# Kernel optimization log

Hardware: AMD Instinct MI355X
Metric: run time of the kernel (lower is better)

Reference implementation:

```python
import jax, jax.numpy as jnp
import numpy as np

N_EMBD = 768
N_HEAD = 12
N_KV_HEAD = 4                      # repeat factor in _repeat_kv
NUM_KV_HEADS = N_HEAD // N_KV_HEAD # 3 actual kv heads
HEAD_DIM = N_EMBD // N_HEAD        # 64
BLOCK_SIZE = 1024                  # sliding window size
SCALE = (HEAD_DIM * N_KV_HEAD / N_HEAD) ** (-0.5)


def _rotary_cos_sin(T, d, dtype):
    inv_freq = 1.0 / (10000.0 ** (jnp.arange(0, d, 2, dtype=jnp.float32) / d))
    t = jnp.arange(T, dtype=jnp.float32)
    freqs = jnp.outer(t, inv_freq)  # (T, d/2)
    return jnp.cos(freqs).astype(dtype)[None, None], jnp.sin(freqs).astype(dtype)[None, None]


def _apply_rotary(x):
    # x: (b, h, T, d)
    T, d = x.shape[2], x.shape[3]
    cos, sin = _rotary_cos_sin(T, d, x.dtype)
    x1, x2 = x[..., : d // 2], x[..., d // 2 :]
    return jnp.concatenate([x1 * cos - x2 * sin, x1 * sin + x2 * cos], axis=-1)


def setup_inputs() -> dict:
    key = jax.random.key(0)
    k0, k1, k2, k3, k4 = jax.random.split(key, 5)
    b, T = 2, 2048
    s = 0.02
    return {
        "hidden_states": jax.random.normal(k0, (b, T, N_EMBD), jnp.float32),
        "Wq": jax.random.normal(k1, (N_HEAD * HEAD_DIM, N_EMBD), jnp.float32) * s,
        "Wk": jax.random.normal(k2, (NUM_KV_HEADS * HEAD_DIM, N_EMBD), jnp.float32) * s,
        "Wv": jax.random.normal(k3, (NUM_KV_HEADS * HEAD_DIM, N_EMBD), jnp.float32) * s,
        "Wo": jax.random.normal(k4, (N_EMBD, N_HEAD * HEAD_DIM), jnp.float32) * s,
    }


def reference(hidden_states, Wq, Wk, Wv, Wo):
    b, T, _ = hidden_states.shape
    q = (hidden_states @ Wq.T).reshape(b, T, N_HEAD, HEAD_DIM).transpose(0, 2, 1, 3)
    k = (hidden_states @ Wk.T).reshape(b, T, NUM_KV_HEADS, HEAD_DIM).transpose(0, 2, 1, 3)
    v = (hidden_states @ Wv.T).reshape(b, T, NUM_KV_HEADS, HEAD_DIM).transpose(0, 2, 1, 3)

    # _repeat_kv: each kv head repeated n_kv_head (=4) times contiguously
    k = jnp.repeat(k, N_KV_HEAD, axis=1)
    v = jnp.repeat(v, N_KV_HEAD, axis=1)

    q = _apply_rotary(q)
    k = _apply_rotary(k)

    # centered sliding-window mask (faithful to per-token loop):
    # window_start = clip(i - W//2, 0, T - W); window is always exactly W wide
    W = BLOCK_SIZE
    i = jnp.arange(T)[:, None]
    j = jnp.arange(T)[None, :]
    start = jnp.clip(i - W // 2, 0, T - W)
    mask = (j >= start) & (j < start + W)  # (T, T)

    scores = jnp.einsum("bhqd,bhkd->bhqk", q, k) * SCALE
    scores = jnp.where(mask[None, None], scores, jnp.finfo(scores.dtype).min)
    attn = jax.nn.softmax(scores, axis=-1)
    out = jnp.einsum("bhqk,bhkd->bhqd", attn, v)  # (b, h, T, d)

    out = out.transpose(0, 2, 1, 3).reshape(b, T, N_EMBD)
    return out @ Wo.T
```

## Files before the change

### kernel.cpp

```cpp
#include <hip/hip_runtime.h>
#include <math.h>

#define T_SEQ 2048
#define E 768
#define WIN 1024
#define KDIM 768
#define HS_SZ ((size_t)4096 * 768)
#define SCALE 0.21650635094610965f

typedef _Float16 f16x8 __attribute__((ext_vector_type(8)));
typedef _Float16 f16x4 __attribute__((ext_vector_type(4)));
typedef float f32x4 __attribute__((ext_vector_type(4)));
typedef __attribute__((address_space(3))) _Float16 lf16;

#define MFMA16(a, b, c) __builtin_amdgcn_mfma_f32_16x16x32_f16(a, b, c, 0, 0, 0)

__device__ __forceinline__ void dma16(const _Float16* g, lf16* l) {
    __builtin_amdgcn_global_load_lds(
        (const __attribute__((address_space(1))) void*)g,
        (__attribute__((address_space(3))) void*)l, 16, 0, 0);
}

__device__ __forceinline__ void cast8(const float* __restrict__ src,
                                      _Float16* __restrict__ dst, int i) {
    float4 a = *(const float4*)&src[i];
    float4 b = *(const float4*)&src[i + 4];
    f16x8 h;
    h[0] = (_Float16)a.x; h[1] = (_Float16)a.y; h[2] = (_Float16)a.z; h[3] = (_Float16)a.w;
    h[4] = (_Float16)b.x; h[5] = (_Float16)b.y; h[6] = (_Float16)b.z; h[7] = (_Float16)b.w;
    *(f16x8*)&dst[i] = h;
}

__global__ __launch_bounds__(256) void prep(
    const float* __restrict__ hs,
    const float* __restrict__ Wq, const float* __restrict__ Wk,
    const float* __restrict__ Wv, const float* __restrict__ Wo,
    _Float16* __restrict__ hs16,
    _Float16* __restrict__ Wq16, _Float16* __restrict__ Wk16,
    _Float16* __restrict__ Wv16, _Float16* __restrict__ Wo16,
    float2* __restrict__ rtab) {
    int tid = blockIdx.x * 256 + threadIdx.x;
    int i = tid * 8;
    if (i < 768 * 768) { cast8(Wq, Wq16, i); cast8(Wo, Wo16, i); }
    if (i < 192 * 768) { cast8(Wk, Wk16, i); cast8(Wv, Wv16, i); }
    cast8(hs, hs16, i);
    if (tid < 2048 * 32) {
        int t = tid >> 5, d = tid & 31;
        float inv = powf(10000.0f, -(float)(2 * d) * (1.0f / 64.0f));
        float s, c;
        sincosf((float)t * inv, &s, &c);
        rtab[tid] = make_float2(c, s);
    }
}

__global__ __launch_bounds__(256) void gemm_qkv(
    const _Float16* __restrict__ A16,
    const _Float16* __restrict__ Wq16, const _Float16* __restrict__ Wk16,
    const _Float16* __restrict__ Wv16, const float2* __restrict__ rtab,
    _Float16* __restrict__ q16, _Float16* __restrict__ k16,
    _Float16* __restrict__ vT16) {
    __shared__ __align__(16) _Float16 As[128 * 128];
    __shared__ __align__(16) _Float16 Bs[64 * 128];
    const int tid = threadIdx.x;
    const int bx = blockIdx.x;
    const int m0 = blockIdx.y * 128;
    const int w = tid >> 6, lane = tid & 63;
    const int mm = lane & 15, quad = lane >> 4;

    const _Float16* bbase; int brb;
    if (bx < 12)      { bbase = Wq16; brb = bx * 64; }
    else if (bx < 15) { bbase = Wk16; brb = (bx - 12) * 64; }
    else              { bbase = Wv16; brb = (bx - 15) * 64; }

    const int rofs4 = lane >> 4;
    const int gs = lane & 15;

    const _Float16* agp[8]; lf16* alp[8];
    #pragma unroll
    for (int j = 0; j < 8; ++j) {
        int c = j * 4 + w;
        int rr = c * 4 + rofs4;
        int glog = gs ^ (rr & 15);
        agp[j] = A16 + (size_t)(m0 + rr) * KDIM + glog * 8;
        alp[j] = ((lf16*)As) + c * 512 + lane * 8;
    }
    const _Float16* bgp[4]; lf16* blp[4];
    #pragma unroll
    for (int j = 0; j < 4; ++j) {
        int c = j * 4 + w;
        int rr = c * 4 + rofs4;
        int glog = gs ^ (rr & 15);
        bgp[j] = bbase + (size_t)(brb + rr) * KDIM + glog * 8;
        blp[j] = ((lf16*)Bs) + c * 512 + lane * 8;
    }

    f32x4 acc[2][4] = {};

    for (int it = 0; it < 6; ++it) {
        const int ke = it * 128;
        __syncthreads();
        #pragma unroll
        for (int j = 0; j < 8; ++j) dma16(agp[j] + ke, alp[j]);
        #pragma unroll
        for (int j = 0; j < 4; ++j) dma16(bgp[j] + ke, blp[j]);
        __syncthreads();
        #pragma unroll
        for (int s = 0; s < 4; ++s) {
            const int gq = ((s * 4 + quad) ^ mm) * 8;
            f16x8 ah[2];
            #pragma unroll
            for (int mt = 0; mt < 2; ++mt)
                ah[mt] = *(const f16x8*)&As[(w * 32 + mt * 16 + mm) * 128 + gq];
            #pragma unroll
            for (int nt = 0; nt < 4; ++nt) {
                f16x8 bh = *(const f16x8*)&Bs[(nt * 16 + mm) * 128 + gq];
                #pragma unroll
                for (int mt = 0; mt < 2; ++mt)
                    acc[mt][nt] = MFMA16(ah[mt], bh, acc[mt][nt]);
            }
        }
    }

    if (bx < 12) {
        #pragma unroll
        for (int mt = 0; mt < 2; ++mt)
            #pragma unroll
            for (int r = 0; r < 4; ++r) {
                int row = m0 + w * 32 + mt * 16 + quad * 4 + r;
                int t = row & (T_SEQ - 1);
                _Float16* dst = &q16[(size_t)row * E + bx * 64 + mm];
                #pragma unroll
                for (int nt = 0; nt < 2; ++nt) {
                    int d = nt * 16 + mm;
                    float2 cs = rtab[t * 32 + d];
                    float x1 = acc[mt][nt][r], x2 = acc[mt][nt + 2][r];
                    dst[nt * 16]       = (_Float16)((x1 * cs.x - x2 * cs.y) * SCALE);
                    dst[(nt + 2) * 16] = (_Float16)((x1 * cs.y + x2 * cs.x) * SCALE);
                }
            }
    } else if (bx < 15) {
        int kvh = bx - 12;
        #pragma unroll
        for (int mt = 0; mt < 2; ++mt)
            #pragma unroll
            for (int r = 0; r < 4; ++r) {
                int row = m0 + w * 32 + mt * 16 + quad * 4 + r;
                int t = row & (T_SEQ - 1);
                int b = row >> 11;
                _Float16* dst = &k16[(((size_t)(b * 3 + kvh)) * T_SEQ + t) * 64 + mm];
                #pragma unroll
                for (int nt = 0; nt < 2; ++nt) {
                    int d = nt * 16 + mm;
                    float2 cs = rtab[t * 32 + d];
                    float x1 = acc[mt][nt][r], x2 = acc[mt][nt + 2][r];
                    dst[nt * 16]       = (_Float16)(x1 * cs.x - x2 * cs.y);
                    dst[(nt + 2) * 16] = (_Float16)(x1 * cs.y + x2 * cs.x);
                }
            }
    } else {
        __syncthreads();
        _Float16 (*vs)[136] = (_Float16 (*)[136])As;
        #pragma unroll
        for (int mt = 0; mt < 2; ++mt)
            #pragma unroll
            for (int nt = 0; nt < 4; ++nt) {
                f16x4 pv;
                #pragma unroll
                for (int r = 0; r < 4; ++r) pv[r] = (_Float16)acc[mt][nt][r];
                *(f16x4*)&vs[nt * 16 + mm][w * 32 + mt * 16 + quad * 4] = pv;
            }
        __syncthreads();
        const int kvh = bx - 15;
        const int b = m0 >> 11, tbase = m0 & (T_SEQ - 1);
        const int tl = (tid & 15) * 8;
        #pragma unroll
        for (int j = 0; j < 4; ++j) {
            int dd = (tid >> 4) + j * 16;
            f16x8 vv = *(const f16x8*)&vs[dd][tl];
            *(f16x8*)&vT16[(((size_t)(b * 3 + kvh)) * 64 + dd) * T_SEQ + tbase + tl] = vv;
        }
    }
}

__global__ __launch_bounds__(256) void gemm_out(
    const _Float16* __restrict__ A16, const _Float16* __restrict__ B16,
    float* __restrict__ C) {
    __shared__ __align__(16) _Float16 As[128 * 128];
    __shared__ __align__(16) _Float16 Bs[64 * 128];
    const int tid = threadIdx.x;
    const int n0 = blockIdx.x * 64;
    const int m0 = blockIdx.y * 128;
    const int w = tid >> 6, lane = tid & 63;
    const int mm = lane & 15, quad = lane >> 4;

    const int rofs4 = lane >> 4;
    const int gs = lane & 15;

    const _Float16* agp[8]; lf16* alp[8];
    #pragma unroll
    for (int j = 0; j < 8; ++j) {
        int c = j * 4 + w;
        int rr = c * 4 + rofs4;
        int glog = gs ^ (rr & 15);
        agp[j] = A16 + (size_t)(m0 + rr) * KDIM + glog * 8;
        alp[j] = ((lf16*)As) + c * 512 + lane * 8;
    }
    const _Float16* bgp[4]; lf16* blp[4];
    #pragma unroll
    for (int j = 0; j < 4; ++j) {
        int c = j * 4 + w;
        int rr = c * 4 + rofs4;
        int glog = gs ^ (rr & 15);
        bgp[j] = B16 + (size_t)(n0 + rr) * KDIM + glog * 8;
        blp[j] = ((lf16*)Bs) + c * 512 + lane * 8;
    }

    f32x4 acc[2][4] = {};

    for (int it = 0; it < 6; ++it) {
        const int ke = it * 128;
        __syncthreads();
        #pragma unroll
        for (int j = 0; j < 8; ++j) dma16(agp[j] + ke, alp[j]);
        #pragma unroll
        for (int j = 0; j < 4; ++j) dma16(bgp[j] + ke, blp[j]);
        __syncthreads();
        #pragma unroll
        for (int s = 0; s < 4; ++s) {
            const int gq = ((s * 4 + quad) ^ mm) * 8;
            f16x8 ah[2];
            #pragma unroll
            for (int mt = 0; mt < 2; ++mt)
                ah[mt] = *(const f16x8*)&As[(w * 32 + mt * 16 + mm) * 128 + gq];
            #pragma unroll
            for (int nt = 0; nt < 4; ++nt) {
                f16x8 bh = *(const f16x8*)&Bs[(nt * 16 + mm) * 128 + gq];
                #pragma unroll
                for (int mt = 0; mt < 2; ++mt)
                    acc[mt][nt] = MFMA16(ah[mt], bh, acc[mt][nt]);
            }
        }
    }

    #pragma unroll
    for (int mt = 0; mt < 2; ++mt)
        #pragma unroll
        for (int r = 0; r < 4; ++r) {
            int row = m0 + w * 32 + mt * 16 + quad * 4 + r;
            float* cp = &C[(size_t)row * 768 + n0 + mm];
            #pragma unroll
            for (int nt = 0; nt < 4; ++nt)
                cp[nt * 16] = acc[mt][nt][r];
        }
}

__global__ __launch_bounds__(256) void attn_mfma(const _Float16* __restrict__ q16,
                                                 const _Float16* __restrict__ k16,
                                                 const _Float16* __restrict__ vT16,
                                                 _Float16* __restrict__ aout16) {
    __shared__ __align__(16) char smem[32768 + 10240];
    _Float16* k_s  = (_Float16*)smem;
    _Float16* vT_s = (_Float16*)(smem + 16384);
    _Float16 (*p_s)[40] = (_Float16(*)[40])(smem + 32768);
    float* ored = (float*)smem;
    float* lred = (float*)(smem + 16384);

    const int b = blockIdx.z, h = blockIdx.y;
    const int i0 = blockIdx.x * 64;
    const int plane = b * 3 + (h >> 2);
    const int tid = threadIdx.x;
    const int w = tid >> 6, lane = tid & 63;
    const int m = lane & 15, quad = lane >> 4;
    const int qh = w & 1, kh = w >> 1;
    const int xm = m & 7;

    int s0 = i0 - 512;      s0 = s0 < 0 ? 0 : (s0 > 1024 ? 1024 : s0);
    int sL = i0 + 63 - 512; sL = sL < 0 ? 0 : (sL > 1024 ? 1024 : sL);
    const int nc = (sL + WIN - s0 + 63) >> 6;

    int start_q[2];
    f16x8 qf[2][2];
    #pragma unroll
    for (int qt = 0; qt < 2; ++qt) {
        int qi = i0 + qh * 32 + qt * 16 + m;
        int sq = qi - 512; sq = sq < 0 ? 0 : (sq > 1024 ? 1024 : sq);
        start_q[qt] = sq;
        const _Float16* qp = &q16[((size_t)(b * T_SEQ + qi)) * E + h * 64 + quad * 8];
        qf[qt][0] = *(const f16x8*)&qp[0];
        qf[qt][1] = *(const f16x8*)&qp[32];
    }

    f32x4 o[2][4] = {};
    float l_run[2] = {0.0f, 0.0f};

    const int rofs = lane >> 3;
    const int glog = (lane & 7) ^ rofs;
    const _Float16* kgb[2]; const _Float16* vgb[2];
    _Float16* klw[2]; _Float16* vlw[2];
    #pragma unroll
    for (int j = 0; j < 2; ++j) {
        int rr = (j * 4 + w) * 8 + rofs;
        kgb[j] = k16 + ((size_t)plane * T_SEQ + rr) * 64 + glog * 8;
        vgb[j] = vT16 + ((size_t)plane * 64 + rr) * T_SEQ + glog * 8;
        klw[j] = k_s + (j * 4 + w) * 512 + lane * 8;
        vlw[j] = vT_s + (j * 4 + w) * 512 + lane * 8;
    }

    f16x8 kr[2], vr[2];
    #pragma unroll
    for (int j = 0; j < 2; ++j) {
        kr[j] = *(const f16x8*)(kgb[j] + (size_t)s0 * 64);
        vr[j] = *(const f16x8*)(vgb[j] + s0);
    }
    #pragma unroll
    for (int j = 0; j < 2; ++j) {
        *(f16x8*)klw[j] = kr[j];
        *(f16x8*)vlw[j] = vr[j];
    }

    for (int ci = 0; ci < nc; ++ci) {
        const int c0 = s0 + ci * 64;
        const int sel = (ci & 1) * 4096;
        __syncthreads();
        if (ci + 1 < nc) {
            const int cn = c0 + 64;
            #pragma unroll
            for (int j = 0; j < 2; ++j) {
                kr[j] = *(const f16x8*)(kgb[j] + (size_t)cn * 64);
                vr[j] = *(const f16x8*)(vgb[j] + cn);
            }
        }

        f32x4 st[2][2] = {};
        #pragma unroll
        for (int s = 0; s < 2; ++s) {
            #pragma unroll
            for (int kt = 0; kt < 2; ++kt) {
                int row = kh * 32 + kt * 16 + m;
                int g = (s * 4 + quad) ^ xm;
                f16x8 a = *(const f16x8*)&k_s[sel + row * 64 + g * 8];
                #pragma unroll
                for (int qt = 0; qt < 2; ++qt)
                    st[kt][qt] = MFMA16(a, qf[qt][s], st[kt][qt]);
            }
        }

        const bool boundary = (c0 < sL) || (c0 + 63 > s0 + 1023);
        if (boundary) {
            #pragma unroll
            for (int kt = 0; kt < 2; ++kt)
                #pragma unroll
                for (int qt = 0; qt < 2; ++qt)
                    #pragma unroll
                    for (int r = 0; r < 4; ++r) {
                        int j = c0 + kh * 32 + kt * 16 + quad * 4 + r;
                        bool valid = (j >= start_q[qt]) && (j < start_q[qt] + WIN);
                        st[kt][qt][r] = valid ? st[kt][qt][r] : -INFINITY;
                    }
        }

        #pragma unroll
        for (int kt = 0; kt < 2; ++kt)
            #pragma unroll
            for (int qt = 0; qt < 2; ++qt) {
                float p0 = __expf(st[kt][qt][0]);
                float p1 = __expf(st[kt][qt][1]);
                float p2 = __expf(st[kt][qt][2]);
                float p3 = __expf(st[kt][qt][3]);
                l_run[qt] += (p0 + p1) + (p2 + p3);
                f16x4 pv = {(_Float16)p0, (_Float16)p1, (_Float16)p2, (_Float16)p3};
                *(f16x4*)&p_s[w * 32 + qt * 16 + m][kt * 16 + quad * 4] = pv;
            }

        f16x8 bp[2];
        #pragma unroll
        for (int qt = 0; qt < 2; ++qt)
            bp[qt] = *(const f16x8*)&p_s[w * 32 + qt * 16 + m][quad * 8];
        #pragma unroll
        for (int mt = 0; mt < 4; ++mt) {
            int g = (kh * 4 + quad) ^ xm;
            f16x8 a = *(const f16x8*)&vT_s[sel + (mt * 16 + m) * 64 + g * 8];
            #pragma unroll
            for (int qt = 0; qt < 2; ++qt)
                o[qt][mt] = MFMA16(a, bp[qt], o[qt][mt]);
        }

        if (ci + 1 < nc) {
            const int ns = ((ci + 1) & 1) * 4096;
            #pragma unroll
            for (int j = 0; j < 2; ++j) {
                *(f16x8*)(klw[j] + ns) = kr[j];
                *(f16x8*)(vlw[j] + ns) = vr[j];
            }
        }
    }

    float l_tot[2];
    #pragma unroll
    for (int qt = 0; qt < 2; ++qt) {
        float l = l_run[qt];
        l += __shfl_xor(l, 16);
        l += __shfl_xor(l, 32);
        l_tot[qt] = l;
    }

    __syncthreads();
    if (kh == 1) {
        #pragma unroll
        for (int qt = 0; qt < 2; ++qt) {
            #pragma unroll
            for (int mt = 0; mt < 4; ++mt) {
                int idx = ((qh * 32 + qt * 16 + m) << 6) + mt * 16 + quad * 4;
                *(float4*)&ored[idx] = *(float4*)&o[qt][mt];
            }
            if (quad == 0) lred[qh * 32 + qt * 16 + m] = l_tot[qt];
        }
    }
    __syncthreads();
    if (kh == 0) {
        #pragma unroll
        for (int qt = 0; qt < 2; ++qt) {
            float rl = 1.0f / (l_tot[qt] + lred[qh * 32 + qt * 16 + m]);
            int qi = i0 + qh * 32 + qt * 16 + m;
            _Float16* op = &aout16[((size_t)(b * T_SEQ + qi)) * E + h * 64];
            #pragma unroll
            for (int mt = 0; mt < 4; ++mt) {
                int idx = ((qh * 32 + qt * 16 + m) << 6) + mt * 16 + quad * 4;
                float4 other = *(float4*)&ored[idx];
                f16x4 hv;
                #pragma unroll
                for (int r = 0; r < 4; ++r)
                    hv[r] = (_Float16)((o[qt][mt][r] + (&other.x)[r]) * rl);
                *(f16x4*)&op[mt * 16 + quad * 4] = hv;
            }
        }
    }
}

extern "C" void kernel_launch(void* const* d_in, const int* in_sizes, int n_in,
                              void* d_out, int out_size, void* d_ws, size_t ws_size,
                              hipStream_t stream) {
    const float* hs = (const float*)d_in[0];
    const float* Wq = (const float*)d_in[1];
    const float* Wk = (const float*)d_in[2];
    const float* Wv = (const float*)d_in[3];
    const float* Wo = (const float*)d_in[4];
    float* out = (float*)d_out;

    _Float16* hs16   = (_Float16*)d_ws;
    _Float16* aout16 = hs16 + HS_SZ;
    _Float16* q16    = aout16 + HS_SZ;
    _Float16* k16    = q16 + HS_SZ;
    _Float16* vT16   = k16 + 6 * 2048 * 64;
    _Float16* Wq16   = vT16 + 6 * 2048 * 64;
    _Float16* Wk16   = Wq16 + 768 * 768;
    _Float16* Wv16   = Wk16 + 192 * 768;
    _Float16* Wo16   = Wv16 + 192 * 768;
    float2*   rtab   = (float2*)(Wo16 + 768 * 768);

    dim3 blk(256);
    prep<<<dim3((int)(HS_SZ / 8 / 256)), blk, 0, stream>>>(hs, Wq, Wk, Wv, Wo,
                                                           hs16, Wq16, Wk16, Wv16, Wo16, rtab);
    gemm_qkv<<<dim3(18, 32), blk, 0, stream>>>(hs16, Wq16, Wk16, Wv16, rtab, q16, k16, vT16);
    attn_mfma<<<dim3(32, 12, 2), blk, 0, stream>>>(q16, k16, vT16, aout16);
    gemm_out<<<dim3(12, 32), blk, 0, stream>>>(aout16, Wo16, out);
}
```

Baseline: 133.2 us.

## Fuse fp32-to-fp16 casts and rotary table into GEMM kernels, drop prep

```diff
diff --git a/kernel.cpp b/kernel.cpp
--- a/kernel.cpp
+++ b/kernel.cpp
@@ -21,42 +21,19 @@
         (__attribute__((address_space(3))) void*)l, 16, 0, 0);
 }
 
-__device__ __forceinline__ void cast8(const float* __restrict__ src,
-                                      _Float16* __restrict__ dst, int i) {
-    float4 a = *(const float4*)&src[i];
-    float4 b = *(const float4*)&src[i + 4];
+__device__ __forceinline__ f16x8 cvt8(const float* __restrict__ p) {
+    float4 a = *(const float4*)p;
+    float4 b = *(const float4*)(p + 4);
     f16x8 h;
     h[0] = (_Float16)a.x; h[1] = (_Float16)a.y; h[2] = (_Float16)a.z; h[3] = (_Float16)a.w;
     h[4] = (_Float16)b.x; h[5] = (_Float16)b.y; h[6] = (_Float16)b.z; h[7] = (_Float16)b.w;
-    *(f16x8*)&dst[i] = h;
-}
-
-__global__ __launch_bounds__(256) void prep(
-    const float* __restrict__ hs,
+    return h;
+}
+
+__global__ __launch_bounds__(256) void gemm_qkv(
+    const float* __restrict__ A32,
     const float* __restrict__ Wq, const float* __restrict__ Wk,
-    const float* __restrict__ Wv, const float* __restrict__ Wo,
-    _Float16* __restrict__ hs16,
-    _Float16* __restrict__ Wq16, _Float16* __restrict__ Wk16,
-    _Float16* __restrict__ Wv16, _Float16* __restrict__ Wo16,
-    float2* __restrict__ rtab) {
-    int tid = blockIdx.x * 256 + threadIdx.x;
-    int i = tid * 8;
-    if (i < 768 * 768) { cast8(Wq, Wq16, i); cast8(Wo, Wo16, i); }
-    if (i < 192 * 768) { cast8(Wk, Wk16, i); cast8(Wv, Wv16, i); }
-    cast8(hs, hs16, i);
-    if (tid < 2048 * 32) {
-        int t = tid >> 5, d = tid & 31;
-        float inv = powf(10000.0f, -(float)(2 * d) * (1.0f / 64.0f));
-        float s, c;
-        sincosf((float)t * inv, &s, &c);
-        rtab[tid] = make_float2(c, s);
-    }
-}
-
-__global__ __launch_bounds__(256) void gemm_qkv(
-    const _Float16* __restrict__ A16,
-    const _Float16* __restrict__ Wq16, const _Float16* __restrict__ Wk16,
-    const _Float16* __restrict__ Wv16, const float2* __restrict__ rtab,
+    const float* __restrict__ Wv,
     _Float16* __restrict__ q16, _Float16* __restrict__ k16,
     _Float16* __restrict__ vT16) {
     __shared__ __align__(16) _Float16 As[128 * 128];
@@ -67,31 +44,31 @@
     const int w = tid >> 6, lane = tid & 63;
     const int mm = lane & 15, quad = lane >> 4;
 
-    const _Float16* bbase; int brb;
-    if (bx < 12)      { bbase = Wq16; brb = bx * 64; }
-    else if (bx < 15) { bbase = Wk16; brb = (bx - 12) * 64; }
-    else              { bbase = Wv16; brb = (bx - 15) * 64; }
+    const float* bbase; int brb;
+    if (bx < 12)      { bbase = Wq; brb = bx * 64; }
+    else if (bx < 15) { bbase = Wk; brb = (bx - 12) * 64; }
+    else              { bbase = Wv; brb = (bx - 15) * 64; }
 
     const int rofs4 = lane >> 4;
     const int gs = lane & 15;
 
-    const _Float16* agp[8]; lf16* alp[8];
+    const float* agp[8]; int aofs[8];
     #pragma unroll
     for (int j = 0; j < 8; ++j) {
         int c = j * 4 + w;
         int rr = c * 4 + rofs4;
         int glog = gs ^ (rr & 15);
-        agp[j] = A16 + (size_t)(m0 + rr) * KDIM + glog * 8;
-        alp[j] = ((lf16*)As) + c * 512 + lane * 8;
-    }
-    const _Float16* bgp[4]; lf16* blp[4];
+        agp[j] = A32 + (size_t)(m0 + rr) * KDIM + glog * 8;
+        aofs[j] = c * 512 + lane * 8;
+    }
+    const float* bgp[4]; int bofs[4];
     #pragma unroll
     for (int j = 0; j < 4; ++j) {
         int c = j * 4 + w;
         int rr = c * 4 + rofs4;
         int glog = gs ^ (rr & 15);
         bgp[j] = bbase + (size_t)(brb + rr) * KDIM + glog * 8;
-        blp[j] = ((lf16*)Bs) + c * 512 + lane * 8;
+        bofs[j] = c * 512 + lane * 8;
     }
 
     f32x4 acc[2][4] = {};
@@ -100,9 +77,11 @@
         const int ke = it * 128;
         __syncthreads();
         #pragma unroll
-        for (int j = 0; j < 8; ++j) dma16(agp[j] + ke, alp[j]);
-        #pragma unroll
-        for (int j = 0; j < 4; ++j) dma16(bgp[j] + ke, blp[j]);
+        for (int j = 0; j < 8; ++j)
+            *(f16x8*)&As[aofs[j]] = cvt8(agp[j] + ke);
+        #pragma unroll
+        for (int j = 0; j < 4; ++j)
+            *(f16x8*)&Bs[bofs[j]] = cvt8(bgp[j] + ke);
         __syncthreads();
         #pragma unroll
         for (int s = 0; s < 4; ++s) {
@@ -121,42 +100,56 @@
         }
     }
 
-    if (bx < 12) {
-        #pragma unroll
-        for (int mt = 0; mt < 2; ++mt)
-            #pragma unroll
-            for (int r = 0; r < 4; ++r) {
-                int row = m0 + w * 32 + mt * 16 + quad * 4 + r;
-                int t = row & (T_SEQ - 1);
-                _Float16* dst = &q16[(size_t)row * E + bx * 64 + mm];
-                #pragma unroll
-                for (int nt = 0; nt < 2; ++nt) {
-                    int d = nt * 16 + mm;
-                    float2 cs = rtab[t * 32 + d];
-                    float x1 = acc[mt][nt][r], x2 = acc[mt][nt + 2][r];
-                    dst[nt * 16]       = (_Float16)((x1 * cs.x - x2 * cs.y) * SCALE);
-                    dst[(nt + 2) * 16] = (_Float16)((x1 * cs.y + x2 * cs.x) * SCALE);
+    if (bx < 15) {
+        const float inv0 = powf(10000.0f, -(float)(2 * mm) * (1.0f / 64.0f));
+        const float inv1 = powf(10000.0f, -(float)(2 * (16 + mm)) * (1.0f / 64.0f));
+        if (bx < 12) {
+            #pragma unroll
+            for (int mt = 0; mt < 2; ++mt)
+                #pragma unroll
+                for (int r = 0; r < 4; ++r) {
+                    int row = m0 + w * 32 + mt * 16 + quad * 4 + r;
+                    int t = row & (T_SEQ - 1);
+                    _Float16* dst = &q16[(size_t)row * E + bx * 64 + mm];
+                    float s0, c0, s1, c1;
+                    sincosf((float)t * inv0, &s0, &c0);
+                    sincosf((float)t * inv1, &s1, &c1);
+                    {
+                        float x1 = acc[mt][0][r], x2 = acc[mt][2][r];
+                        dst[0]  = (_Float16)((x1 * c0 - x2 * s0) * SCALE);
+                        dst[32] = (_Float16)((x1 * s0 + x2 * c0) * SCALE);
+                    }
+                    {
+                        float x1 = acc[mt][1][r], x2 = acc[mt][3][r];
+                        dst[16] = (_Float16)((x1 * c1 - x2 * s1) * SCALE);
+                        dst[48] = (_Float16)((x1 * s1 + x2 * c1) * SCALE);
+                    }
                 }
-            }
-    } else if (bx < 15) {
-        int kvh = bx - 12;
-        #pragma unroll
-        for (int mt = 0; mt < 2; ++mt)
-            #pragma unroll
-            for (int r = 0; r < 4; ++r) {
-                int row = m0 + w * 32 + mt * 16 + quad * 4 + r;
-                int t = row & (T_SEQ - 1);
-                int b = row >> 11;
-                _Float16* dst = &k16[(((size_t)(b * 3 + kvh)) * T_SEQ + t) * 64 + mm];
-                #pragma unroll
-                for (int nt = 0; nt < 2; ++nt) {
-                    int d = nt * 16 + mm;
-                    float2 cs = rtab[t * 32 + d];
-                    float x1 = acc[mt][nt][r], x2 = acc[mt][nt + 2][r];
-                    dst[nt * 16]       = (_Float16)(x1 * cs.x - x2 * cs.y);
-                    dst[(nt + 2) * 16] = (_Float16)(x1 * cs.y + x2 * cs.x);
+        } else {
+            int kvh = bx - 12;
+            #pragma unroll
+            for (int mt = 0; mt < 2; ++mt)
+                #pragma unroll
+                for (int r = 0; r < 4; ++r) {
+                    int row = m0 + w * 32 + mt * 16 + quad * 4 + r;
+                    int t = row & (T_SEQ - 1);
+                    int b = row >> 11;
+                    _Float16* dst = &k16[(((size_t)(b * 3 + kvh)) * T_SEQ + t) * 64 + mm];
+                    float s0, c0, s1, c1;
+                    sincosf((float)t * inv0, &s0, &c0);
+                    sincosf((float)t * inv1, &s1, &c1);
+                    {
+                        float x1 = acc[mt][0][r], x2 = acc[mt][2][r];
+                        dst[0]  = (_Float16)(x1 * c0 - x2 * s0);
+                        dst[32] = (_Float16)(x1 * s0 + x2 * c0);
+                    }
+                    {
+                        float x1 = acc[mt][1][r], x2 = acc[mt][3][r];
+                        dst[16] = (_Float16)(x1 * c1 - x2 * s1);
+                        dst[48] = (_Float16)(x1 * s1 + x2 * c1);
+                    }
                 }
-            }
+        }
     } else {
         __syncthreads();
         _Float16 (*vs)[136] = (_Float16 (*)[136])As;
@@ -183,7 +176,7 @@
 }
 
 __global__ __launch_bounds__(256) void gemm_out(
-    const _Float16* __restrict__ A16, const _Float16* __restrict__ B16,
+    const _Float16* __restrict__ A16, const float* __restrict__ B32,
     float* __restrict__ C) {
     __shared__ __align__(16) _Float16 As[128 * 128];
     __shared__ __align__(16) _Float16 Bs[64 * 128];
@@ -205,14 +198,14 @@
         agp[j] = A16 + (size_t)(m0 + rr) * KDIM + glog * 8;
         alp[j] = ((lf16*)As) + c * 512 + lane * 8;
     }
-    const _Float16* bgp[4]; lf16* blp[4];
+    const float* bgp[4]; int bofs[4];
     #pragma unroll
     for (int j = 0; j < 4; ++j) {
         int c = j * 4 + w;
         int rr = c * 4 + rofs4;
         int glog = gs ^ (rr & 15);
-        bgp[j] = B16 + (size_t)(n0 + rr) * KDIM + glog * 8;
-        blp[j] = ((lf16*)Bs) + c * 512 + lane * 8;
+        bgp[j] = B32 + (size_t)(n0 + rr) * KDIM + glog * 8;
+        bofs[j] = c * 512 + lane * 8;
     }
 
     f32x4 acc[2][4] = {};
@@ -223,7 +216,8 @@
         #pragma unroll
         for (int j = 0; j < 8; ++j) dma16(agp[j] + ke, alp[j]);
         #pragma unroll
-        for (int j = 0; j < 4; ++j) dma16(bgp[j] + ke, blp[j]);
+        for (int j = 0; j < 4; ++j)
+            *(f16x8*)&Bs[bofs[j]] = cvt8(bgp[j] + ke);
         __syncthreads();
         #pragma unroll
         for (int s = 0; s < 4; ++s) {
@@ -447,21 +441,13 @@
     const float* Wo = (const float*)d_in[4];
     float* out = (float*)d_out;
 
-    _Float16* hs16   = (_Float16*)d_ws;
-    _Float16* aout16 = hs16 + HS_SZ;
+    _Float16* aout16 = (_Float16*)d_ws;
     _Float16* q16    = aout16 + HS_SZ;
     _Float16* k16    = q16 + HS_SZ;
     _Float16* vT16   = k16 + 6 * 2048 * 64;
-    _Float16* Wq16   = vT16 + 6 * 2048 * 64;
-    _Float16* Wk16   = Wq16 + 768 * 768;
-    _Float16* Wv16   = Wk16 + 192 * 768;
-    _Float16* Wo16   = Wv16 + 192 * 768;
-    float2*   rtab   = (float2*)(Wo16 + 768 * 768);
 
     dim3 blk(256);
-    prep<<<dim3((int)(HS_SZ / 8 / 256)), blk, 0, stream>>>(hs, Wq, Wk, Wv, Wo,
-                                                           hs16, Wq16, Wk16, Wv16, Wo16, rtab);
-    gemm_qkv<<<dim3(18, 32), blk, 0, stream>>>(hs16, Wq16, Wk16, Wv16, rtab, q16, k16, vT16);
+    gemm_qkv<<<dim3(18, 32), blk, 0, stream>>>(hs, Wq, Wk, Wv, q16, k16, vT16);
     attn_mfma<<<dim3(32, 12, 2), blk, 0, stream>>>(q16, k16, vT16, aout16);
-    gemm_out<<<dim3(12, 32), blk, 0, stream>>>(aout16, Wo16, out);
-}
+    gemm_out<<<dim3(12, 32), blk, 0, stream>>>(aout16, Wo, out);
+}
```

New measurement: 148.4 us. 1.11x slower.
